# Kernel optimization log

Measured on AMD Instinct MI355X. Metric: run time of the kernel, lower is better.

The kernel has to match this reference:

```python
import jax, jax.numpy as jnp
import numpy as np

N_NODES = 100000
N_EDGES = 1600000
D_IN, D_HID, D_OUT = 128, 128, 64


def setup_inputs() -> dict:
    key = jax.random.key(0)
    ks = jax.random.split(key, 8)
    x = jax.random.normal(ks[0], (N_NODES, D_IN), dtype=jnp.float32)
    edge_index = jax.random.randint(ks[1], (2, N_EDGES), 0, N_NODES, dtype=jnp.int64)
    def glorot(k, fan_in, fan_out):
        s = jnp.sqrt(6.0 / (fan_in + fan_out))
        return jax.random.uniform(k, (fan_in, fan_out), jnp.float32, -s, s)
    return {
        "x": x,
        "edge_index": edge_index,
        "W1": glorot(ks[2], D_IN, D_HID), "b1": jnp.zeros((D_HID,), jnp.float32),
        "W2": glorot(ks[3], D_HID, D_HID), "b2": jnp.zeros((D_HID,), jnp.float32),
        "W3": glorot(ks[4], D_HID, D_OUT), "b3": jnp.zeros((D_OUT,), jnp.float32),
    }


def _gcn_norm(edge_index, n_nodes):
    # add self-loops, compute symmetric normalization D^-1/2 A D^-1/2
    loop = jnp.arange(n_nodes, dtype=edge_index.dtype)
    src = jnp.concatenate([edge_index[0], loop])  # message source
    dst = jnp.concatenate([edge_index[1], loop])  # aggregation target
    deg = jax.ops.segment_sum(jnp.ones_like(dst, dtype=jnp.float32), dst,
                              num_segments=n_nodes)
    dinv = jnp.where(deg > 0, jax.lax.rsqrt(deg), 0.0)
    norm = dinv[src] * dinv[dst]  # [E + N]
    return src, dst, norm


def _gcn_conv(x, W, b, src, dst, norm, n_nodes):
    xw = x @ W                                # dense transform [N, F_out]
    msg = xw[src] * norm[:, None]             # gather + scale   [E+N, F_out]
    out = jax.ops.segment_sum(msg, dst, num_segments=n_nodes)  # scatter-add
    return out + b


def reference(x, edge_index, W1, b1, W2, b2, W3, b3):
    n = x.shape[0]
    src, dst, norm = _gcn_norm(edge_index, n)  # cached=True: same norm reused
    h = jax.nn.relu(_gcn_conv(x, W1, b1, src, dst, norm, n))
    h = jax.nn.relu(_gcn_conv(h, W2, b2, src, dst, norm, n))
    return _gcn_conv(h, W3, b3, src, dst, norm, n)
```

## Files before the change

kernel.cpp:

```cpp
#include <hip/hip_runtime.h>
#include <hip/hip_fp16.h>


#define NN 100000
#define NE 1600000
#define TT (NE + NN)
#define BSH 9
#define NBUCK ((NN + 511) / 512)
#define EPB1 16384
#define NPB1 ((TT + EPB1 - 1) / EPB1)

typedef _Float16 f16x8 __attribute__((ext_vector_type(8)));
typedef float f32x4 __attribute__((ext_vector_type(4)));


__global__ __launch_bounds__(256) void bucket_count(const int* __restrict__ ei,
                                                    int* __restrict__ gbc) {
    __shared__ int hist[NBUCK];
    const int tid = threadIdx.x;
    const int base = blockIdx.x * EPB1;
    for (int b = tid; b < NBUCK; b += 256) hist[b] = 0;
    __syncthreads();
    for (int i = tid; i < EPB1; i += 256) {
        int e = base + i;
        if (e >= TT) break;
        int d = (e < NE) ? ei[NE + e] : (e - NE);
        atomicAdd(&hist[d >> BSH], 1);
    }
    __syncthreads();
    for (int b = tid; b < NBUCK; b += 256)
        if (hist[b]) atomicAdd(&gbc[b], hist[b]);
}


__global__ __launch_bounds__(256) void scan_buckets(const int* __restrict__ gbc,
                                                    int* __restrict__ bbase,
                                                    int* __restrict__ gcursor,
                                                    int* __restrict__ rowptr) {
    __shared__ int s[256];
    const int t = threadIdx.x;
    int v = (t < NBUCK) ? gbc[t] : 0;
    s[t] = v;
    __syncthreads();
    for (int off = 1; off < 256; off <<= 1) {
        int u = (t >= off) ? s[t - off] : 0;
        __syncthreads();
        s[t] += u;
        __syncthreads();
    }
    if (t < NBUCK) {
        int excl = s[t] - v;
        bbase[t] = excl;
        gcursor[t] = excl;
    }
    if (t == 0) { bbase[NBUCK] = TT; rowptr[NN] = TT; }
}


__global__ __launch_bounds__(256) void partition_p1(const int* __restrict__ ei,
                                                    int* __restrict__ gcursor,
                                                    int* __restrict__ part) {
    __shared__ int hist[NBUCK];
    const int tid = threadIdx.x;
    const int base = blockIdx.x * EPB1;
    for (int b = tid; b < NBUCK; b += 256) hist[b] = 0;
    __syncthreads();
    for (int i = tid; i < EPB1; i += 256) {
        int e = base + i;
        if (e >= TT) break;
        int d = (e < NE) ? ei[NE + e] : (e - NE);
        atomicAdd(&hist[d >> BSH], 1);
    }
    __syncthreads();
    for (int b = tid; b < NBUCK; b += 256) {
        int cnt = hist[b];
        hist[b] = cnt ? atomicAdd(&gcursor[b], cnt) : 0;
    }
    __syncthreads();
    for (int i = tid; i < EPB1; i += 256) {
        int e = base + i;
        if (e >= TT) break;
        int s, d;
        if (e < NE) { s = ei[e]; d = ei[NE + e]; }
        else        { s = d = e - NE; }
        int pos = atomicAdd(&hist[d >> BSH], 1);
        part[pos] = s | ((d & 511) << 17);
    }
}


__global__ __launch_bounds__(256) void partition_p2(const int* __restrict__ part,
                                                    const int* __restrict__ bbase,
                                                    int* __restrict__ rowptr,
                                                    float* __restrict__ dinv,
                                                    int* __restrict__ col) {
    __shared__ int cnt[512];
    __shared__ int scn[512];
    __shared__ int cur[512];
    const int b = blockIdx.x;
    const int v0 = b << BSH;
    const int nv = min(512, NN - v0);
    const int tid = threadIdx.x;
    const int base = bbase[b];
    const int nrec = bbase[b + 1] - base;

    cnt[tid] = 0; cnt[tid + 256] = 0;
    __syncthreads();
    for (int i = tid; i < nrec; i += 256)
        atomicAdd(&cnt[((unsigned)part[base + i]) >> 17], 1);
    __syncthreads();
    scn[tid] = cnt[tid]; scn[tid + 256] = cnt[tid + 256];
    __syncthreads();
    for (int off = 1; off < 512; off <<= 1) {
        int a = (tid >= off) ? scn[tid - off] : 0;
        int c = (tid + 256 >= off) ? scn[tid + 256 - off] : 0;
        __syncthreads();
        scn[tid] += a; scn[tid + 256] += c;
        __syncthreads();
    }
#pragma unroll
    for (int p = 0; p < 2; p++) {
        int j = tid + p * 256;
        if (j < nv) {
            int excl = scn[j] - cnt[j];
            rowptr[v0 + j] = base + excl;
            dinv[v0 + j] = rsqrtf((float)cnt[j]);
            cur[j] = base + excl;
        }
    }
    __syncthreads();
    for (int i = tid; i < nrec; i += 256) {
        int r = part[base + i];
        int pos = atomicAdd(&cur[((unsigned)r) >> 17], 1);
        col[pos] = r & 0x1FFFF;
    }
}


__global__ __launch_bounds__(256) void wt_conv_all(const float* __restrict__ W1,
                                                   const float* __restrict__ W2,
                                                   const float* __restrict__ W3,
                                                   _Float16* __restrict__ Wt1,
                                                   _Float16* __restrict__ Wt2,
                                                   _Float16* __restrict__ Wt3) {
    int idx = blockIdx.x * 256 + threadIdx.x;
    if (idx < 16384) {
        Wt1[(idx % 128) * 128 + idx / 128] = (_Float16)W1[idx];
    } else if (idx < 32768) {
        int i = idx - 16384;
        Wt2[(i % 128) * 128 + i / 128] = (_Float16)W2[i];
    } else if (idx < 40960) {
        int i = idx - 32768;
        Wt3[(i % 64) * 128 + i / 64] = (_Float16)W3[i];
    }
}


template <int F, bool AHALF>
__global__ __launch_bounds__(256) void gemm_mfma(const void* __restrict__ Ap,
                                                 const _Float16* __restrict__ Wt,
                                                 const float* __restrict__ dinv,
                                                 __half* __restrict__ Yh) {
    constexpr int NT = F / 16;
    __shared__ _Float16 Yl[64][136];

    const int tid = threadIdx.x;
    const int wave = tid >> 6;
    const int lane = tid & 63;
    const int m = lane & 15;
    const int q = lane >> 4;
    const int grow0 = blockIdx.x * 64;
    const int row = grow0 + wave * 16 + m;
    const bool rok = row < NN;

    f32x4 acc[NT];
#pragma unroll
    for (int t = 0; t < NT; t++) acc[t] = (f32x4){0.f, 0.f, 0.f, 0.f};

#pragma unroll
    for (int kt = 0; kt < 128; kt += 32) {
        const int k0 = kt + q * 8;
        union { f16x8 v; _Float16 e[8]; } au;
        if (rok) {
            if constexpr (AHALF) {
                au.v = *reinterpret_cast<const f16x8*>(
                    (const __half*)Ap + (size_t)row * 128 + k0);
            } else {
                const float* A = (const float*)Ap;
                float4 x0 = *reinterpret_cast<const float4*>(A + (size_t)row * 128 + k0);
                float4 x1 = *reinterpret_cast<const float4*>(A + (size_t)row * 128 + k0 + 4);
                au.e[0] = (_Float16)x0.x; au.e[1] = (_Float16)x0.y;
                au.e[2] = (_Float16)x0.z; au.e[3] = (_Float16)x0.w;
                au.e[4] = (_Float16)x1.x; au.e[5] = (_Float16)x1.y;
                au.e[6] = (_Float16)x1.z; au.e[7] = (_Float16)x1.w;
            }
        } else {
#pragma unroll
            for (int j = 0; j < 8; j++) au.e[j] = (_Float16)0.f;
        }
#pragma unroll
        for (int t = 0; t < NT; t++) {
            f16x8 bf = *reinterpret_cast<const f16x8*>(Wt + (t * 16 + m) * 128 + k0);
            acc[t] = __builtin_amdgcn_mfma_f32_16x16x32_f16(au.v, bf, acc[t], 0, 0, 0);
        }
    }
#pragma unroll
    for (int r = 0; r < 4; r++) {
        int lrow = wave * 16 + q * 4 + r;
        int gr = grow0 + lrow;
        float s = (gr < NN) ? dinv[gr] : 0.f;
#pragma unroll
        for (int t = 0; t < NT; t++)
            Yl[lrow][t * 16 + m] = (_Float16)(s * acc[t][r]);
    }
    __syncthreads();
    constexpr int CH = F / 8;
    for (int i = tid; i < 64 * CH; i += 256) {
        int lrow = i / CH, c = i % CH;
        int gr = grow0 + lrow;
        if (gr < NN)
            *reinterpret_cast<f16x8*>(Yh + (size_t)gr * F + c * 8) =
                *reinterpret_cast<const f16x8*>(&Yl[lrow][c * 8]);
    }
}


__device__ __forceinline__ void acc_add8(float* acc, float4 raw) {
    const __half2* h2 = reinterpret_cast<const __half2*>(&raw);
#pragma unroll
    for (int qq = 0; qq < 4; qq++) {
        float2 fv = __half22float2(h2[qq]);
        acc[2 * qq]     += fv.x;
        acc[2 * qq + 1] += fv.y;
    }
}


template <int FOUT>
__global__ __launch_bounds__(256) void fused_agg_gemm(
        const __half* __restrict__ XWh,
        const int* __restrict__ rowptr,
        const int* __restrict__ col,
        const float* __restrict__ dinv,
        const float* __restrict__ bias,
        const _Float16* __restrict__ Wt,
        __half* __restrict__ Yout) {
    __shared__ _Float16 Hs[16][136];
    __shared__ _Float16 Ds[16][FOUT + 8];

    const int tid = threadIdx.x;
    const int v0 = blockIdx.x * 16;

    {
        const int lnode = tid >> 4;
        const int f = tid & 15;
        const int v = v0 + lnode;
        const int beg = rowptr[v];
        const int end = rowptr[v + 1];
        const float4* base = reinterpret_cast<const float4*>(XWh);
        float acc[8] = {0.f, 0.f, 0.f, 0.f, 0.f, 0.f, 0.f, 0.f};
#pragma unroll 4
        for (int e = beg; e < end; e++) {
            int u = col[e];
            float4 raw = base[(size_t)u * 16 + f];
            acc_add8(acc, raw);
        }
        const float dv = dinv[v];
        union { f16x8 v8; _Float16 e8[8]; } hu;
#pragma unroll
        for (int qq = 0; qq < 8; qq++) {
            float r = dv * acc[qq] + bias[f * 8 + qq];
            hu.e8[qq] = (_Float16)fmaxf(r, 0.f);
        }
        *reinterpret_cast<f16x8*>(&Hs[lnode][f * 8]) = hu.v8;
    }
    __syncthreads();

    constexpr int TPW = FOUT / 64;
    const int wave = tid >> 6;
    const int lane = tid & 63;
    const int m = lane & 15;
    const int q = lane >> 4;
    f32x4 gacc[TPW];
#pragma unroll
    for (int t = 0; t < TPW; t++) gacc[t] = (f32x4){0.f, 0.f, 0.f, 0.f};
#pragma unroll
    for (int kt = 0; kt < 128; kt += 32) {
        const int k0 = kt + q * 8;
        f16x8 av = *reinterpret_cast<const f16x8*>(&Hs[m][k0]);
#pragma unroll
        for (int t = 0; t < TPW; t++) {
            const int gc = (wave * TPW + t) * 16 + m;
            f16x8 bv = *reinterpret_cast<const f16x8*>(Wt + gc * 128 + k0);
            gacc[t] = __builtin_amdgcn_mfma_f32_16x16x32_f16(av, bv, gacc[t], 0, 0, 0);
        }
    }
#pragma unroll
    for (int r = 0; r < 4; r++) {
        const int lrow = q * 4 + r;
        const float s = dinv[v0 + lrow];
#pragma unroll
        for (int t = 0; t < TPW; t++)
            Ds[lrow][(wave * TPW + t) * 16 + m] = (_Float16)(s * gacc[t][r]);
    }
    __syncthreads();
    constexpr int CH = FOUT / 8;
    for (int i2 = tid; i2 < 16 * CH; i2 += 256) {
        int lrow = i2 / CH, c = i2 % CH;
        *reinterpret_cast<f16x8*>(Yout + (size_t)(v0 + lrow) * FOUT + c * 8) =
            *reinterpret_cast<const f16x8*>(&Ds[lrow][c * 8]);
    }
}


__global__ __launch_bounds__(256) void agg_final(
        const __half* __restrict__ XWh,
        const int* __restrict__ rowptr,
        const int* __restrict__ col,
        const float* __restrict__ dinv,
        const float* __restrict__ bias,
        float* __restrict__ out) {
    constexpr int TPN = 8;
    constexpr int NPB = 256 / TPN;
    const int v = blockIdx.x * NPB + threadIdx.x / TPN;
    const int f = threadIdx.x % TPN;
    const int beg = rowptr[v];
    const int end = rowptr[v + 1];
    const float4* base = reinterpret_cast<const float4*>(XWh);
    float acc[8] = {0.f, 0.f, 0.f, 0.f, 0.f, 0.f, 0.f, 0.f};
#pragma unroll 4
    for (int e = beg; e < end; e++) {
        int u = col[e];
        float4 raw = base[(size_t)u * TPN + f];
        acc_add8(acc, raw);
    }
    const float dv = dinv[v];
    float r[8];
#pragma unroll
    for (int q = 0; q < 8; q++)
        r[q] = dv * acc[q] + bias[f * 8 + q];
    float* op = out + (size_t)v * 64 + f * 8;
    *reinterpret_cast<float4*>(op)     = make_float4(r[0], r[1], r[2], r[3]);
    *reinterpret_cast<float4*>(op + 4) = make_float4(r[4], r[5], r[6], r[7]);
}


extern "C" void kernel_launch(void* const* d_in, const int* in_sizes, int n_in,
                              void* d_out, int out_size, void* d_ws, size_t ws_size,
                              hipStream_t stream) {
    const float* x  = (const float*)d_in[0];
    const int*   ei = (const int*)d_in[1];
    const float* W1 = (const float*)d_in[2];
    const float* b1 = (const float*)d_in[3];
    const float* W2 = (const float*)d_in[4];
    const float* b2 = (const float*)d_in[5];
    const float* W3 = (const float*)d_in[6];
    const float* b3 = (const float*)d_in[7];
    float* out = (float*)d_out;

    char* p = (char*)d_ws;
    int*      rowptr  = (int*)p;       p += 400016;
    float*    dinv    = (float*)p;     p += 400000;
    int*      gbc     = (int*)p;       p += 1024;
    int*      bbase   = (int*)p;       p += 1024;
    int*      gcursor = (int*)p;       p += 1024;
    _Float16* Wt1     = (_Float16*)p;  p += 32768;
    _Float16* Wt2     = (_Float16*)p;  p += 32768;
    _Float16* Wt3     = (_Float16*)p;  p += 16384;
    int*      part    = (int*)p;       p += (size_t)TT * 4;
    int*      col     = (int*)p;       p += (size_t)TT * 4;
    __half*   xwh1    = (__half*)p;    p += (size_t)NN * 128 * 2;
    __half*   xwh2    = (__half*)p;
    __half*   xwh3    = xwh1;

    hipMemsetAsync(gbc, 0, NBUCK * 4, stream);
    wt_conv_all<<<160, 256, 0, stream>>>(W1, W2, W3, Wt1, Wt2, Wt3);
    bucket_count<<<NPB1, 256, 0, stream>>>(ei, gbc);
    scan_buckets<<<1, 256, 0, stream>>>(gbc, bbase, gcursor, rowptr);
    partition_p1<<<NPB1, 256, 0, stream>>>(ei, gcursor, part);
    partition_p2<<<NBUCK, 256, 0, stream>>>(part, bbase, rowptr, dinv, col);

    const int gb = (NN + 63) / 64;
    const int fb = NN / 16;
    gemm_mfma<128, false><<<gb, 256, 0, stream>>>(x, Wt1, dinv, xwh1);
    fused_agg_gemm<128><<<fb, 256, 0, stream>>>(xwh1, rowptr, col, dinv, b1,
                                                Wt2, xwh2);
    fused_agg_gemm<64><<<fb, 256, 0, stream>>>(xwh2, rowptr, col, dinv, b2,
                                               Wt3, xwh3);
    agg_final<<<NN / 32, 256, 0, stream>>>(xwh3, rowptr, col, dinv, b3, out);
}
```

Before: 455.8 us.

## Fold memset and bucket scan into neighbor kernels, shrink partition chunks

Moves the bucket-count zeroing into the weight-conversion kernel and merges the single-block scan into bucket_count using a last-block-done atomic counter, removing a memset and a kernel launch. The edges-per-block for the partition passes is reduced from 16384 to 2048, giving many more blocks so the count and scatter passes spread across more CUs. partition_p2 now runs 512 threads, one per vertex slot. The trade-offs are more global atomics on the bucket counters and a threadfence-based completion protocol.

```diff
diff --git a/kernel.cpp b/kernel.cpp
--- a/kernel.cpp
+++ b/kernel.cpp
@@ -7,16 +7,45 @@
 #define TT (NE + NN)
 #define BSH 9
 #define NBUCK ((NN + 511) / 512)
-#define EPB1 16384
+#define EPB1 2048
 #define NPB1 ((TT + EPB1 - 1) / EPB1)
 
 typedef _Float16 f16x8 __attribute__((ext_vector_type(8)));
 typedef float f32x4 __attribute__((ext_vector_type(4)));
 
 
+__global__ __launch_bounds__(256) void wt_conv_all(const float* __restrict__ W1,
+                                                   const float* __restrict__ W2,
+                                                   const float* __restrict__ W3,
+                                                   _Float16* __restrict__ Wt1,
+                                                   _Float16* __restrict__ Wt2,
+                                                   _Float16* __restrict__ Wt3,
+                                                   int* __restrict__ gbc,
+                                                   int* __restrict__ done,
+                                                   int* __restrict__ bbase,
+                                                   int* __restrict__ rowptr) {
+    int idx = blockIdx.x * 256 + threadIdx.x;
+    if (idx < 16384) {
+        Wt1[(idx % 128) * 128 + idx / 128] = (_Float16)W1[idx];
+    } else if (idx < 32768) {
+        int i = idx - 16384;
+        Wt2[(i % 128) * 128 + i / 128] = (_Float16)W2[i];
+    } else if (idx < 40960) {
+        int i = idx - 32768;
+        Wt3[(i % 64) * 128 + i / 64] = (_Float16)W3[i];
+    }
+    if (idx < NBUCK) gbc[idx] = 0;
+    if (idx == 0) { *done = 0; bbase[NBUCK] = TT; rowptr[NN] = TT; }
+}
+
+
 __global__ __launch_bounds__(256) void bucket_count(const int* __restrict__ ei,
-                                                    int* __restrict__ gbc) {
+                                                    int* __restrict__ gbc,
+                                                    int* __restrict__ done,
+                                                    int* __restrict__ bbase,
+                                                    int* __restrict__ gcursor) {
     __shared__ int hist[NBUCK];
+    __shared__ int amlast;
     const int tid = threadIdx.x;
     const int base = blockIdx.x * EPB1;
     for (int b = tid; b < NBUCK; b += 256) hist[b] = 0;
@@ -30,30 +59,29 @@
     __syncthreads();
     for (int b = tid; b < NBUCK; b += 256)
         if (hist[b]) atomicAdd(&gbc[b], hist[b]);
-}
-
-
-__global__ __launch_bounds__(256) void scan_buckets(const int* __restrict__ gbc,
-                                                    int* __restrict__ bbase,
-                                                    int* __restrict__ gcursor,
-                                                    int* __restrict__ rowptr) {
-    __shared__ int s[256];
-    const int t = threadIdx.x;
-    int v = (t < NBUCK) ? gbc[t] : 0;
-    s[t] = v;
-    __syncthreads();
-    for (int off = 1; off < 256; off <<= 1) {
-        int u = (t >= off) ? s[t - off] : 0;
+    __threadfence();
+    if (tid == 0) amlast = (atomicAdd(done, 1) == (int)gridDim.x - 1);
+    __syncthreads();
+    if (amlast) {
+        __threadfence();
+        __shared__ int s[256];
+        int v = (tid < NBUCK)
+            ? __hip_atomic_load(&gbc[tid], __ATOMIC_RELAXED,
+                                __HIP_MEMORY_SCOPE_AGENT) : 0;
+        s[tid] = v;
         __syncthreads();
-        s[t] += u;
-        __syncthreads();
-    }
-    if (t < NBUCK) {
-        int excl = s[t] - v;
-        bbase[t] = excl;
-        gcursor[t] = excl;
-    }
-    if (t == 0) { bbase[NBUCK] = TT; rowptr[NN] = TT; }
+        for (int off = 1; off < 256; off <<= 1) {
+            int u = (tid >= off) ? s[tid - off] : 0;
+            __syncthreads();
+            s[tid] += u;
+            __syncthreads();
+        }
+        if (tid < NBUCK) {
+            int excl = s[tid] - v;
+            bbase[tid] = excl;
+            gcursor[tid] = excl;
+        }
+    }
 }
 
 
@@ -89,7 +117,7 @@
 }
 
 
-__global__ __launch_bounds__(256) void partition_p2(const int* __restrict__ part,
+__global__ __launch_bounds__(512) void partition_p2(const int* __restrict__ part,
                                                     const int* __restrict__ bbase,
                                                     int* __restrict__ rowptr,
                                                     float* __restrict__ dinv,
@@ -104,54 +132,30 @@
     const int base = bbase[b];
     const int nrec = bbase[b + 1] - base;
 
-    cnt[tid] = 0; cnt[tid + 256] = 0;
-    __syncthreads();
-    for (int i = tid; i < nrec; i += 256)
+    cnt[tid] = 0;
+    __syncthreads();
+    for (int i = tid; i < nrec; i += 512)
         atomicAdd(&cnt[((unsigned)part[base + i]) >> 17], 1);
     __syncthreads();
-    scn[tid] = cnt[tid]; scn[tid + 256] = cnt[tid + 256];
+    scn[tid] = cnt[tid];
     __syncthreads();
     for (int off = 1; off < 512; off <<= 1) {
         int a = (tid >= off) ? scn[tid - off] : 0;
-        int c = (tid + 256 >= off) ? scn[tid + 256 - off] : 0;
         __syncthreads();
-        scn[tid] += a; scn[tid + 256] += c;
+        scn[tid] += a;
         __syncthreads();
     }
-#pragma unroll
-    for (int p = 0; p < 2; p++) {
-        int j = tid + p * 256;
-        if (j < nv) {
-            int excl = scn[j] - cnt[j];
-            rowptr[v0 + j] = base + excl;
-            dinv[v0 + j] = rsqrtf((float)cnt[j]);
-            cur[j] = base + excl;
-        }
-    }
-    __syncthreads();
-    for (int i = tid; i < nrec; i += 256) {
+    if (tid < nv) {
+        int excl = scn[tid] - cnt[tid];
+        rowptr[v0 + tid] = base + excl;
+        dinv[v0 + tid] = rsqrtf((float)cnt[tid]);
+        cur[tid] = base + excl;
+    }
+    __syncthreads();
+    for (int i = tid; i < nrec; i += 512) {
         int r = part[base + i];
         int pos = atomicAdd(&cur[((unsigned)r) >> 17], 1);
         col[pos] = r & 0x1FFFF;
-    }
-}
-
-
-__global__ __launch_bounds__(256) void wt_conv_all(const float* __restrict__ W1,
-                                                   const float* __restrict__ W2,
-                                                   const float* __restrict__ W3,
-                                                   _Float16* __restrict__ Wt1,
-                                                   _Float16* __restrict__ Wt2,
-                                                   _Float16* __restrict__ Wt3) {
-    int idx = blockIdx.x * 256 + threadIdx.x;
-    if (idx < 16384) {
-        Wt1[(idx % 128) * 128 + idx / 128] = (_Float16)W1[idx];
-    } else if (idx < 32768) {
-        int i = idx - 16384;
-        Wt2[(i % 128) * 128 + i / 128] = (_Float16)W2[i];
-    } else if (idx < 40960) {
-        int i = idx - 32768;
-        Wt3[(i % 64) * 128 + i / 64] = (_Float16)W3[i];
     }
 }
 
@@ -364,6 +368,7 @@
     int*      gbc     = (int*)p;       p += 1024;
     int*      bbase   = (int*)p;       p += 1024;
     int*      gcursor = (int*)p;       p += 1024;
+    int*      done    = (int*)p;       p += 1024;
     _Float16* Wt1     = (_Float16*)p;  p += 32768;
     _Float16* Wt2     = (_Float16*)p;  p += 32768;
     _Float16* Wt3     = (_Float16*)p;  p += 16384;
@@ -373,12 +378,11 @@
     __half*   xwh2    = (__half*)p;
     __half*   xwh3    = xwh1;
 
-    hipMemsetAsync(gbc, 0, NBUCK * 4, stream);
-    wt_conv_all<<<160, 256, 0, stream>>>(W1, W2, W3, Wt1, Wt2, Wt3);
-    bucket_count<<<NPB1, 256, 0, stream>>>(ei, gbc);
-    scan_buckets<<<1, 256, 0, stream>>>(gbc, bbase, gcursor, rowptr);
+    wt_conv_all<<<160, 256, 0, stream>>>(W1, W2, W3, Wt1, Wt2, Wt3,
+                                         gbc, done, bbase, rowptr);
+    bucket_count<<<NPB1, 256, 0, stream>>>(ei, gbc, done, bbase, gcursor);
     partition_p1<<<NPB1, 256, 0, stream>>>(ei, gcursor, part);
-    partition_p2<<<NBUCK, 256, 0, stream>>>(part, bbase, rowptr, dinv, col);
+    partition_p2<<<NBUCK, 512, 0, stream>>>(part, bbase, rowptr, dinv, col);
 
     const int gb = (NN + 63) / 64;
     const int fb = NN / 16;
```

New measurement: 471.4 us. +3.4%, slower.
